# Optimization experiments

Hardware: AMD Instinct MI355X
Metric: run time of the kernel (lower is better)

Reference implementation:

```python
import jax, jax.numpy as jnp
import numpy as np

ROLE_BITS = 20
NHEAD = 16
D_MODEL = 1024
D_KEY = D_MODEL // NHEAD  # 64
D_FIL = 512
DFF = 4096
EPS = 1e-5


def _ln(x, g, b):
    mu = jnp.mean(x, axis=-1, keepdims=True)
    var = jnp.mean(jnp.square(x - mu), axis=-1, keepdims=True)
    return (x - mu) * jax.lax.rsqrt(var + EPS) * g + b


def setup_inputs() -> dict:
    key = jax.random.key(0)
    ks = jax.random.split(key, 10)
    N, BSZ, MEM = 16384, 16, 8
    D_IN = D_FIL + ROLE_BITS  # 532
    values = jax.random.normal(ks[0], (N, D_FIL), jnp.float32)
    role_index = jax.random.randint(ks[1], (N,), 1, 2 ** ROLE_BITS)
    # every (batch, memory_slot) pair occupied -> static shapes (compression is a no-op)
    slot = jax.random.permutation(ks[2], jnp.tile(jnp.arange(BSZ * MEM), N // (BSZ * MEM)))
    batch_index = (slot // MEM).astype(jnp.int32)
    memory_index = (slot % MEM).astype(jnp.int32)
    query_vectors = jax.random.normal(ks[3], (NHEAD, D_KEY), jnp.float32) * (1.0 / np.sqrt(D_KEY))
    s = 0.02
    Wk = jax.random.normal(ks[4], (D_MODEL, D_IN), jnp.float32) * s
    Wv = jax.random.normal(ks[5], (D_MODEL, D_IN), jnp.float32) * s
    Wo = jax.random.normal(ks[6], (D_MODEL, D_MODEL), jnp.float32) * s
    W1 = jax.random.normal(ks[7], (DFF, D_MODEL), jnp.float32) * s
    W2 = jax.random.normal(ks[8], (D_MODEL, DFF), jnp.float32) * s
    return dict(
        values=values, role_index=role_index, batch_index=batch_index,
        memory_index=memory_index, query_vectors=query_vectors,
        Wk=Wk, Wv=Wv, Wo=Wo, bo=jnp.zeros((D_MODEL,), jnp.float32),
        W1=W1, b1=jnp.zeros((DFF,), jnp.float32),
        W2=W2, b2=jnp.zeros((D_MODEL,), jnp.float32),
        g_fil=jnp.ones((D_FIL,), jnp.float32), b_fil=jnp.zeros((D_FIL,), jnp.float32),
        g_mha=jnp.ones((D_IN,), jnp.float32), b_mha=jnp.zeros((D_IN,), jnp.float32),
        g_ff=jnp.ones((D_MODEL,), jnp.float32), b_ff=jnp.zeros((D_MODEL,), jnp.float32),
        g_out=jnp.ones((D_MODEL,), jnp.float32), b_out=jnp.zeros((D_MODEL,), jnp.float32),
        bsz=BSZ, memory_slots=MEM,
    )


def _tree_positional_encodings(role_index):
    # bit-expand role indices: column j is bit j of the role index
    bits = (jnp.bitwise_and(role_index[:, None], 2 ** jnp.arange(ROLE_BITS)) != 0).astype(jnp.float32)
    # locate the highest set bit (torch: flip + argmax)
    mi = jnp.argmax(bits[:, ::-1], axis=1)
    cm = ROLE_BITS - 1 - mi  # index of highest set bit
    bits = bits * (1.0 - jax.nn.one_hot(cm, ROLE_BITS, dtype=bits.dtype))  # zero it out
    branch = jnp.arange(ROLE_BITS)[None, :] < cm[:, None]
    return jnp.where(branch, (bits - 0.5) * 2.0, bits)  # {0,1} -> {-1,1} below MSB


def reference(values, role_index, batch_index, memory_index, query_vectors,
              Wk, Wv, Wo, bo, W1, b1, W2, b2,
              g_fil, b_fil, g_mha, b_mha, g_ff, b_ff, g_out, b_out,
              bsz, memory_slots):
    N = values.shape[0]
    T = bsz * memory_slots  # num_trees (all (batch, slot) pairs occupied)

    tpd = _tree_positional_encodings(role_index)
    x = jnp.concatenate([_ln(values, g_fil, b_fil), tpd], axis=1)  # [N, d_input]
    x = _ln(x, g_mha, b_mha)
    k = (x @ Wk.T).reshape(N, NHEAD, D_KEY)
    v = (x @ Wv.T).reshape(N, NHEAD, D_KEY)
    qkm = jnp.einsum('nhd,hd->nh', k, query_vectors)  # [N, H]

    # combined batch+memory mask: node n attends to flat tree t = b*mem + m
    node_slot = batch_index * memory_slots + memory_index  # [N]
    mask = node_slot[:, None] == jnp.arange(T)[None, :]  # [N, T]
    scores = jnp.where(mask[:, :, None], qkm[:, None, :], -1e9) / np.sqrt(D_KEY)
    attn = jax.nn.softmax(scores, axis=0)  # softmax over nodes, [N, T, H]
    out = jnp.einsum('nhv,nth->thv', v, attn).reshape(T, D_MODEL)

    # post-attention: proj_o + residual with flattened queries, LN, FF, LN
    r1 = (out @ Wo.T + bo) + query_vectors.reshape(-1)
    l1 = _ln(r1, g_ff, b_ff)
    ff = jax.nn.gelu(l1 @ W1.T + b1, approximate=False) @ W2.T + b2
    l2 = _ln(ff + r1, g_out, b_out)

    rectangle_out = l2.reshape(bsz, memory_slots, D_MODEL)
    agent_pad_mask = jnp.zeros((bsz, memory_slots), dtype=bool)
    return rectangle_out, agent_pad_mask
```

## Files before the change

kernel.cpp:

```cpp
#include <hip/hip_runtime.h>
#include <hip/hip_bf16.h>

typedef __hip_bfloat16 bf16;

#define N_NODES 16384
#define D_FIL 512
#define D_IN 532
#define D_MODEL 1024
#define NHEAD 16
#define D_KEY 64
#define DFF 4096
#define NTREE 128
#define MEM_SLOTS 8
#define NODES_PER_TREE 128
#define EPS 1e-5f
#define XSE 544
#define XSU 272
#define CSTR 32
#define BSTR 40

typedef float f32x4 __attribute__((ext_vector_type(4)));
typedef short s16x8 __attribute__((ext_vector_type(8)));

union PackU { uint4 u; s16x8 s; };

__device__ inline float gelu_exact(float x) {
    return 0.5f * x * (1.0f + erff(x * 0.7071067811865476f));
}

__device__ inline void blockReduceSum2_512(float& a, float& b, float* sm) {
    int tid = threadIdx.x;
    int lane = tid & 63, wid = tid >> 6;
#pragma unroll
    for (int off = 32; off > 0; off >>= 1) {
        a += __shfl_down(a, off, 64);
        b += __shfl_down(b, off, 64);
    }
    if (lane == 0) { sm[wid] = a; sm[8 + wid] = b; }
    __syncthreads();
    if (tid == 0) {
        float s0 = 0.f, s1 = 0.f;
#pragma unroll
        for (int i = 0; i < 8; ++i) { s0 += sm[i]; s1 += sm[8 + i]; }
        sm[16] = s0; sm[17] = s1;
    }
    __syncthreads();
    a = sm[16]; b = sm[17];
}

__global__ __launch_bounds__(256) void prep_kernel(
        const float* __restrict__ values, const int* __restrict__ role,
        const int* __restrict__ bidx, const int* __restrict__ midx,
        const float* __restrict__ g_fil, const float* __restrict__ b_fil,
        const float* __restrict__ g_mha, const float* __restrict__ b_mha,
        bf16* __restrict__ xs, int* __restrict__ counts,
        const float* __restrict__ q, const float* __restrict__ Wk,
        unsigned* __restrict__ wqb,
        const float* __restrict__ Wv, float* __restrict__ wvt) {
    int b = blockIdx.x;
    int tid = threadIdx.x;

    if (b < 16) {
        int h = b;
        __shared__ float qs[64];
        if (tid < 64) qs[tid] = q[h * 64 + tid];
        __syncthreads();
        for (int p = tid; p < XSU; p += 256) {
            unsigned out = 0u;
            if (p < 266) {
                float a0 = 0.f, a1 = 0.f;
                int j0 = 2 * p;
#pragma unroll 8
                for (int d = 0; d < 64; ++d) {
                    const float* wr = Wk + (size_t)(h * 64 + d) * D_IN;
                    a0 += qs[d] * wr[j0];
                    a1 += qs[d] * wr[j0 + 1];
                }
                unsigned u0 = (unsigned)__bfloat16_as_ushort(__float2bfloat16(a0));
                unsigned u1 = (unsigned)__bfloat16_as_ushort(__float2bfloat16(a1));
                out = (u1 << 16) | u0;
            }
            wqb[h * XSU + p] = out;
        }
        return;
    }

    if (b < 560) {
        __shared__ float tile[32][33];
        int vb = b - 16;
        int c0 = (vb & 31) * 32, j0 = (vb >> 5) * 32;
        int tx = tid & 31, ty = tid >> 5;
#pragma unroll
        for (int r = 0; r < 4; ++r) {
            int cc = ty + r * 8;
            int j = j0 + tx;
            tile[cc][tx] = (j < D_IN) ? Wv[(size_t)(c0 + cc) * D_IN + j] : 0.f;
        }
        __syncthreads();
#pragma unroll
        for (int r = 0; r < 4; ++r) {
            int j = j0 + ty + r * 8;
            if (j < D_IN) wvt[(size_t)j * D_MODEL + c0 + tx] = tile[tx][ty + r * 8];
        }
        return;
    }

    int wave = tid >> 6;
    int l = tid & 63;
    int n = (b - 560) * 4 + wave;

    const float4* vp = (const float4*)(values + (size_t)n * D_FIL + l * 8);
    float4 v0 = vp[0], v1 = vp[1];

    int row = 0;
    if (l == 0) {
        int slot = bidx[n] * MEM_SLOTS + midx[n];
        int pos = atomicAdd(&counts[slot * CSTR], 1);
        row = slot * NODES_PER_TREE + pos;
    }

    float s = v0.x + v0.y + v0.z + v0.w + v1.x + v1.y + v1.z + v1.w;
    float ss = v0.x * v0.x + v0.y * v0.y + v0.z * v0.z + v0.w * v0.w
             + v1.x * v1.x + v1.y * v1.y + v1.z * v1.z + v1.w * v1.w;
#pragma unroll
    for (int m = 1; m < 64; m <<= 1) {
        s += __shfl_xor(s, m, 64);
        ss += __shfl_xor(ss, m, 64);
    }
    float mu = s * (1.f / D_FIL);
    float var = ss * (1.f / D_FIL) - mu * mu;
    float rs = rsqrtf(var + EPS);

    const float4* gf = (const float4*)(g_fil + l * 8);
    const float4* bf = (const float4*)(b_fil + l * 8);
    float4 gf0 = gf[0], gf1 = gf[1], bf0 = bf[0], bf1 = bf[1];
    float y[8];
    y[0] = (v0.x - mu) * rs * gf0.x + bf0.x;
    y[1] = (v0.y - mu) * rs * gf0.y + bf0.y;
    y[2] = (v0.z - mu) * rs * gf0.z + bf0.z;
    y[3] = (v0.w - mu) * rs * gf0.w + bf0.w;
    y[4] = (v1.x - mu) * rs * gf1.x + bf1.x;
    y[5] = (v1.y - mu) * rs * gf1.y + bf1.y;
    y[6] = (v1.z - mu) * rs * gf1.z + bf1.z;
    y[7] = (v1.w - mu) * rs * gf1.w + bf1.w;

    int r = role[n];
    int cm = 31 - __clz(r);
    float s_t = 2.f * (float)(__popc(r) - 1) - (float)cm;
    float ss_t = (float)cm;

    float s2 = y[0] + y[1] + y[2] + y[3] + y[4] + y[5] + y[6] + y[7];
    float ss2 = y[0] * y[0] + y[1] * y[1] + y[2] * y[2] + y[3] * y[3]
              + y[4] * y[4] + y[5] * y[5] + y[6] * y[6] + y[7] * y[7];
#pragma unroll
    for (int m = 1; m < 64; m <<= 1) {
        s2 += __shfl_xor(s2, m, 64);
        ss2 += __shfl_xor(ss2, m, 64);
    }
    s2 += s_t; ss2 += ss_t;
    float mu2 = s2 * (1.f / D_IN);
    float var2 = ss2 * (1.f / D_IN) - mu2 * mu2;
    float rs2 = rsqrtf(var2 + EPS);

    const float4* gm = (const float4*)(g_mha + l * 8);
    const float4* bm = (const float4*)(b_mha + l * 8);
    float4 gm0 = gm[0], gm1 = gm[1], bm0 = bm[0], bm1 = bm[1];
    float x[8];
    x[0] = (y[0] - mu2) * rs2 * gm0.x + bm0.x;
    x[1] = (y[1] - mu2) * rs2 * gm0.y + bm0.y;
    x[2] = (y[2] - mu2) * rs2 * gm0.z + bm0.z;
    x[3] = (y[3] - mu2) * rs2 * gm0.w + bm0.w;
    x[4] = (y[4] - mu2) * rs2 * gm1.x + bm1.x;
    x[5] = (y[5] - mu2) * rs2 * gm1.y + bm1.y;
    x[6] = (y[6] - mu2) * rs2 * gm1.z + bm1.z;
    x[7] = (y[7] - mu2) * rs2 * gm1.w + bm1.w;

    row = __shfl(row, 0, 64);

    {
        unsigned us[8];
#pragma unroll
        for (int k = 0; k < 8; ++k)
            us[k] = (unsigned)__bfloat16_as_ushort(__float2bfloat16(x[k]));
        uint4 pk = make_uint4((us[1] << 16) | us[0], (us[3] << 16) | us[2],
                              (us[5] << 16) | us[4], (us[7] << 16) | us[6]);
        *(uint4*)((char*)xs + (size_t)row * (XSE * 2) + 16 * l) = pk;
    }

    if (l < 20) {
        int bit = (r >> l) & 1;
        float tpd = (l < cm) ? (bit ? 1.f : -1.f) : 0.f;
        float x2 = (tpd - mu2) * rs2 * g_mha[512 + l] + b_mha[512 + l];
        xs[(size_t)row * XSE + 512 + l] = __float2bfloat16(x2);
    } else if (l < 26) {
        ((unsigned*)xs)[(size_t)row * XSU + 266 + (l - 20)] = 0u;
    }
}

__global__ __launch_bounds__(256) void attn_fused_kernel(const unsigned* __restrict__ xsu,
                                                         const unsigned* __restrict__ wqb,
                                                         const float* __restrict__ wvt,
                                                         float* __restrict__ attn_out) {
    int hg = blockIdx.x, t = blockIdx.y, tid = threadIdx.x;
    __shared__ __align__(16) float a4[NODES_PER_TREE * 4];
    __shared__ __align__(16) char sbuf[8576];
    unsigned* wsh = (unsigned*)sbuf;
    float (*zs)[536] = (float(*)[536])sbuf;

    for (int i = tid; i < 4 * 274; i += 256) {
        int hh = i / 274, p = i - hh * 274;
        wsh[hh * 274 + p] = (p < XSU) ? wqb[(hg * 4 + hh) * XSU + p] : 0u;
    }
    __syncthreads();

    {
        int i = tid >> 2, hh = tid & 3;
        const uint2* xr0 = (const uint2*)(xsu + (size_t)(t * NODES_PER_TREE + i) * XSU);
        const uint2* xr1 = (const uint2*)(xsu + (size_t)(t * NODES_PER_TREE + i + 64) * XSU);
        const uint2* wr  = (const uint2*)(wsh + hh * 274);
        float a0 = 0.f, a1 = 0.f;
#pragma unroll 8
        for (int j = 0; j < 133; ++j) {
            uint2 wu = wr[j];
            uint2 xa = xr0[j];
            uint2 xb = xr1[j];
            float w0 = __uint_as_float(wu.x << 16), w1 = __uint_as_float(wu.x & 0xffff0000u);
            float w2 = __uint_as_float(wu.y << 16), w3 = __uint_as_float(wu.y & 0xffff0000u);
            a0 += __uint_as_float(xa.x << 16) * w0 + __uint_as_float(xa.x & 0xffff0000u) * w1
                + __uint_as_float(xa.y << 16) * w2 + __uint_as_float(xa.y & 0xffff0000u) * w3;
            a1 += __uint_as_float(xb.x << 16) * w0 + __uint_as_float(xb.x & 0xffff0000u) * w1
                + __uint_as_float(xb.y << 16) * w2 + __uint_as_float(xb.y & 0xffff0000u) * w3;
        }
        a4[tid] = a0 * 0.125f;
        a4[tid + 256] = a1 * 0.125f;
    }
    __syncthreads();

    int hh = tid >> 6, lane = tid & 63;
    {
        float s0 = a4[lane * 4 + hh], s1 = a4[(lane + 64) * 4 + hh];
        float m = fmaxf(s0, s1);
#pragma unroll
        for (int off = 32; off > 0; off >>= 1) m = fmaxf(m, __shfl_xor(m, off, 64));
        float e0 = expf(s0 - m), e1 = expf(s1 - m);
        float sum = e0 + e1;
#pragma unroll
        for (int off = 32; off > 0; off >>= 1) sum += __shfl_xor(sum, off, 64);
        float inv = 1.0f / sum;
        a4[lane * 4 + hh] = e0 * inv;
        a4[(lane + 64) * 4 + hh] = e1 * inv;
    }
    __syncthreads();

    {
        bool hasT = tid < 10;
        float az[4][2] = {};
        float at[4][2] = {};
        const unsigned* xt = xsu + (size_t)t * NODES_PER_TREE * XSU;
        for (int i0 = 0; i0 < NODES_PER_TREE; i0 += 8) {
            unsigned u[8], u2[8];
            float4 av[8];
#pragma unroll
            for (int k = 0; k < 8; ++k) u[k] = xt[(size_t)(i0 + k) * XSU + tid];
#pragma unroll
            for (int k = 0; k < 8; ++k) u2[k] = hasT ? xt[(size_t)(i0 + k) * XSU + 256 + tid] : 0u;
#pragma unroll
            for (int k = 0; k < 8; ++k) av[k] = *(const float4*)(a4 + (i0 + k) * 4);
#pragma unroll
            for (int k = 0; k < 8; ++k) {
                float x0 = __uint_as_float(u[k] << 16);
                float x1 = __uint_as_float(u[k] & 0xffff0000u);
                float x2 = __uint_as_float(u2[k] << 16);
                float x3 = __uint_as_float(u2[k] & 0xffff0000u);
                float4 a = av[k];
                az[0][0] += a.x * x0; az[0][1] += a.x * x1;
                az[1][0] += a.y * x0; az[1][1] += a.y * x1;
                az[2][0] += a.z * x0; az[2][1] += a.z * x1;
                az[3][0] += a.w * x0; az[3][1] += a.w * x1;
                at[0][0] += a.x * x2; at[0][1] += a.x * x3;
                at[1][0] += a.y * x2; at[1][1] += a.y * x3;
                at[2][0] += a.z * x2; at[2][1] += a.z * x3;
                at[3][0] += a.w * x2; at[3][1] += a.w * x3;
            }
        }
        __syncthreads();
#pragma unroll
        for (int k = 0; k < 4; ++k) {
            *(float2*)(&zs[k][2 * tid]) = make_float2(az[k][0], az[k][1]);
            if (hasT) *(float2*)(&zs[k][512 + 2 * tid]) = make_float2(at[k][0], at[k][1]);
        }
    }
    __syncthreads();

    int c = hg * 256 + tid;
    const float* wp = wvt + c;
    float acc0 = 0.f, acc1 = 0.f;
    for (int j0 = 0; j0 < 528; j0 += 8) {
        float wv[8];
#pragma unroll
        for (int k = 0; k < 8; ++k) wv[k] = wp[(size_t)(j0 + k) * D_MODEL];
#pragma unroll
        for (int k = 0; k < 8; k += 2) {
            acc0 += zs[hh][j0 + k] * wv[k];
            acc1 += zs[hh][j0 + k + 1] * wv[k + 1];
        }
    }
    {
        float wv[4];
#pragma unroll
        for (int k = 0; k < 4; ++k) wv[k] = wp[(size_t)(528 + k) * D_MODEL];
#pragma unroll
        for (int k = 0; k < 4; k += 2) {
            acc0 += zs[hh][528 + k] * wv[k];
            acc1 += zs[hh][528 + k + 1] * wv[k + 1];
        }
    }
    attn_out[(size_t)t * D_MODEL + c] = acc0 + acc1;
}

__global__ __launch_bounds__(256) void gemm_mfma_sk(const float* __restrict__ A,
                                                    const float* __restrict__ B,
                                                    float* __restrict__ Cpart,
                                                    int N, int K, int nsb) {
    __shared__ __align__(16) unsigned short bhi[32 * BSTR];
    __shared__ __align__(16) unsigned short blo[32 * BSTR];
    int tid = threadIdx.x;
    int col0 = blockIdx.x * 32;
    int k0 = blockIdx.y * nsb * 32;
    float* C = Cpart + (size_t)blockIdx.y * 128 * N;

    int w = tid >> 6, l = tid & 63;
    int l15 = l & 15, l4 = l >> 4;
    int scol = tid >> 3, sk4 = (tid & 7) * 4;

    f32x4 acc[2][2];
#pragma unroll
    for (int rt = 0; rt < 2; ++rt)
#pragma unroll
        for (int ct = 0; ct < 2; ++ct) acc[rt][ct] = (f32x4){0.f, 0.f, 0.f, 0.f};

    for (int s = 0; s < nsb; ++s) {
        int kb = k0 + s * 32;

        const float* bp = B + (size_t)(col0 + scol) * K + kb + sk4;
        float4 fb = *(const float4*)bp;

        float4 fa[2][2];
#pragma unroll
        for (int rt = 0; rt < 2; ++rt) {
            const float* ap = A + (size_t)(32 * w + 16 * rt + l15) * K + kb + l4 * 8;
            fa[rt][0] = *(const float4*)ap;
            fa[rt][1] = *(const float4*)(ap + 4);
        }

        {
            float fe[4] = {fb.x, fb.y, fb.z, fb.w};
            unsigned hu[2], lu[2];
#pragma unroll
            for (int p = 0; p < 2; ++p) {
                unsigned u0 = __float_as_uint(fe[2 * p]);
                unsigned u1 = __float_as_uint(fe[2 * p + 1]);
                unsigned h0 = u0 & 0xffff0000u, h1 = u1 & 0xffff0000u;
                float d0 = fe[2 * p] - __uint_as_float(h0);
                float d1 = fe[2 * p + 1] - __uint_as_float(h1);
                hu[p] = h1 | (u0 >> 16);
                lu[p] = (__float_as_uint(d1) & 0xffff0000u) | (__float_as_uint(d0) >> 16);
            }
            *(uint2*)(&bhi[scol * BSTR + sk4]) = make_uint2(hu[0], hu[1]);
            *(uint2*)(&blo[scol * BSTR + sk4]) = make_uint2(lu[0], lu[1]);
        }
        __syncthreads();

        s16x8 ah[2], al[2];
#pragma unroll
        for (int rt = 0; rt < 2; ++rt) {
            float fe[8] = {fa[rt][0].x, fa[rt][0].y, fa[rt][0].z, fa[rt][0].w,
                           fa[rt][1].x, fa[rt][1].y, fa[rt][1].z, fa[rt][1].w};
            unsigned hu[4], lu[4];
#pragma unroll
            for (int p = 0; p < 4; ++p) {
                unsigned u0 = __float_as_uint(fe[2 * p]);
                unsigned u1 = __float_as_uint(fe[2 * p + 1]);
                unsigned h0 = u0 & 0xffff0000u, h1 = u1 & 0xffff0000u;
                float d0 = fe[2 * p] - __uint_as_float(h0);
                float d1 = fe[2 * p + 1] - __uint_as_float(h1);
                hu[p] = h1 | (u0 >> 16);
                lu[p] = (__float_as_uint(d1) & 0xffff0000u) | (__float_as_uint(d0) >> 16);
            }
            PackU uh, ul;
            uh.u = make_uint4(hu[0], hu[1], hu[2], hu[3]);
            ul.u = make_uint4(lu[0], lu[1], lu[2], lu[3]);
            ah[rt] = uh.s;
            al[rt] = ul.s;
        }

#pragma unroll
        for (int ct = 0; ct < 2; ++ct) {
            PackU rbh, rbl;
            rbh.u = *(const uint4*)(&bhi[(16 * ct + l15) * BSTR + l4 * 8]);
            rbl.u = *(const uint4*)(&blo[(16 * ct + l15) * BSTR + l4 * 8]);
#pragma unroll
            for (int rt = 0; rt < 2; ++rt) {
                acc[rt][ct] = __builtin_amdgcn_mfma_f32_16x16x32_bf16(ah[rt], rbh.s, acc[rt][ct], 0, 0, 0);
                acc[rt][ct] = __builtin_amdgcn_mfma_f32_16x16x32_bf16(al[rt], rbh.s, acc[rt][ct], 0, 0, 0);
                acc[rt][ct] = __builtin_amdgcn_mfma_f32_16x16x32_bf16(ah[rt], rbl.s, acc[rt][ct], 0, 0, 0);
            }
        }
        __syncthreads();
    }

#pragma unroll
    for (int rt = 0; rt < 2; ++rt) {
        int row = 32 * w + 16 * rt + l4 * 4;
#pragma unroll
        for (int ct = 0; ct < 2; ++ct) {
            int col = col0 + 16 * ct + l15;
#pragma unroll
            for (int r = 0; r < 4; ++r)
                C[(size_t)(row + r) * N + col] = acc[rt][ct][r];
        }
    }
}

__global__ __launch_bounds__(512) void ln_r1_kernel(const float* __restrict__ po, const float* __restrict__ bo,
                             const float* __restrict__ qvec, const float* __restrict__ g,
                             const float* __restrict__ b, float* __restrict__ r1,
                             float* __restrict__ l1) {
    int t = blockIdx.x, tid = threadIdx.x;
    __shared__ float sm[18];
    float e[2];
#pragma unroll
    for (int c = 0; c < 2; ++c) {
        int j = c * 512 + tid;
        float v = bo[j] + qvec[j];
#pragma unroll
        for (int s = 0; s < 8; ++s)
            v += po[(size_t)s * NTREE * D_MODEL + (size_t)t * D_MODEL + j];
        e[c] = v;
        r1[(size_t)t * D_MODEL + j] = v;
    }
    float s = e[0] + e[1];
    float ss = e[0] * e[0] + e[1] * e[1];
    blockReduceSum2_512(s, ss, sm);
    float mu = s * (1.f / D_MODEL);
    float var = ss * (1.f / D_MODEL) - mu * mu;
    float rs = rsqrtf(var + EPS);
#pragma unroll
    for (int c = 0; c < 2; ++c) {
        int j = c * 512 + tid;
        l1[(size_t)t * D_MODEL + j] = (e[c] - mu) * rs * g[j] + b[j];
    }
}

__global__ void gelu_reduce_kernel(const float* __restrict__ p1, const float* __restrict__ b1,
                                   float* __restrict__ h1) {
    int idx4 = (blockIdx.x * 256 + threadIdx.x) * 4;
    int col = idx4 & (DFF - 1);
    float4 v = *(const float4*)(b1 + col);
#pragma unroll
    for (int s = 0; s < 4; ++s) {
        float4 p = *(const float4*)(p1 + (size_t)s * NTREE * DFF + idx4);
        v.x += p.x; v.y += p.y; v.z += p.z; v.w += p.w;
    }
    v.x = gelu_exact(v.x); v.y = gelu_exact(v.y);
    v.z = gelu_exact(v.z); v.w = gelu_exact(v.w);
    *(float4*)(h1 + idx4) = v;
}

__global__ __launch_bounds__(512) void ln_out_kernel(const float* __restrict__ p2, const float* __restrict__ b2,
                              const float* __restrict__ r1, const float* __restrict__ g,
                              const float* __restrict__ b, float* __restrict__ out) {
    int t = blockIdx.x, tid = threadIdx.x;
    __shared__ float sm[18];
    float e[2];
#pragma unroll
    for (int c = 0; c < 2; ++c) {
        int j = c * 512 + tid;
        float v = b2[j] + r1[(size_t)t * D_MODEL + j];
#pragma unroll
        for (int s = 0; s < 16; ++s)
            v += p2[(size_t)s * NTREE * D_MODEL + (size_t)t * D_MODEL + j];
        e[c] = v;
    }
    float s = e[0] + e[1];
    float ss = e[0] * e[0] + e[1] * e[1];
    blockReduceSum2_512(s, ss, sm);
    float mu = s * (1.f / D_MODEL);
    float var = ss * (1.f / D_MODEL) - mu * mu;
    float rs = rsqrtf(var + EPS);
#pragma unroll
    for (int c = 0; c < 2; ++c) {
        int j = c * 512 + tid;
        out[(size_t)t * D_MODEL + j] = (e[c] - mu) * rs * g[j] + b[j];
    }
    if (t == 0 && tid < 128) out[(size_t)NTREE * D_MODEL + tid] = 0.f;
}

extern "C" void kernel_launch(void* const* d_in, const int* in_sizes, int n_in,
                              void* d_out, int out_size, void* d_ws, size_t ws_size,
                              hipStream_t stream) {
    const float* values = (const float*)d_in[0];
    const int* role     = (const int*)d_in[1];
    const int* bidx     = (const int*)d_in[2];
    const int* midx     = (const int*)d_in[3];
    const float* qvec   = (const float*)d_in[4];
    const float* Wk     = (const float*)d_in[5];
    const float* Wv     = (const float*)d_in[6];
    const float* Wo     = (const float*)d_in[7];
    const float* bo     = (const float*)d_in[8];
    const float* W1     = (const float*)d_in[9];
    const float* b1     = (const float*)d_in[10];
    const float* W2     = (const float*)d_in[11];
    const float* b2     = (const float*)d_in[12];
    const float* g_fil  = (const float*)d_in[13];
    const float* b_fil  = (const float*)d_in[14];
    const float* g_mha  = (const float*)d_in[15];
    const float* b_mha  = (const float*)d_in[16];
    const float* g_ff   = (const float*)d_in[17];
    const float* b_ff   = (const float*)d_in[18];
    const float* g_out  = (const float*)d_in[19];
    const float* b_out  = (const float*)d_in[20];

    char* w = (char*)d_ws;
    int*   counts   = (int*)(w + 0);
    unsigned* wqb   = (unsigned*)(w + 16384);
    float* attn_out = (float*)(w + 34816);
    float* r1       = (float*)(w + 559104);
    float* l1       = (float*)(w + 1083392);
    float* h1       = (float*)(w + 1607680);
    float* wvt      = (float*)(w + 3704832);
    char*  big      = w + 5883904;
    bf16*  xs = (bf16*)big;
    float* po = (float*)big;
    float* p1 = (float*)(big + 4194304);
    float* p2 = (float*)big;

    float* out = (float*)d_out;

    hipMemsetAsync(counts, 0, 16384, stream);

    prep_kernel<<<4656, 256, 0, stream>>>(values, role, bidx, midx,
                                          g_fil, b_fil, g_mha, b_mha,
                                          xs, counts,
                                          qvec, Wk, wqb, Wv, wvt);

    attn_fused_kernel<<<dim3(4, NTREE), 256, 0, stream>>>((const unsigned*)xs, wqb, wvt, attn_out);

    gemm_mfma_sk<<<dim3(32, 8), 256, 0, stream>>>(attn_out, Wo, po, D_MODEL, D_MODEL, 4);

    ln_r1_kernel<<<NTREE, 512, 0, stream>>>(po, bo, qvec, g_ff, b_ff, r1, l1);

    gemm_mfma_sk<<<dim3(128, 4), 256, 0, stream>>>(l1, W1, p1, DFF, D_MODEL, 8);

    gelu_reduce_kernel<<<512, 256, 0, stream>>>(p1, b1, h1);

    gemm_mfma_sk<<<dim3(32, 16), 256, 0, stream>>>(h1, W2, p2, D_MODEL, DFF, 8);

    ln_out_kernel<<<NTREE, 512, 0, stream>>>(p2, b2, r1, g_out, b_out, out);
}
```

Before: 236.6 us.

## Double attention kernel block size and remap blocks so trees share an XCD

The fused attention kernel now runs 512 threads per block. Each thread computes one score, the weighted value sum is split across two node halves and reduced in shared memory, and the Wv projection is split across two K halves. The 1D grid is remapped so the four head-groups of a tree land on the same XCD, which should improve L2 reuse of that tree's activations. The cost is more shared memory, extra barriers and reduction passes, and idle threads during the softmax.

```diff
diff --git a/kernel.cpp b/kernel.cpp
--- a/kernel.cpp
+++ b/kernel.cpp
@@ -197,17 +197,21 @@
     }
 }
 
-__global__ __launch_bounds__(256) void attn_fused_kernel(const unsigned* __restrict__ xsu,
+__global__ __launch_bounds__(512) void attn_fused_kernel(const unsigned* __restrict__ xsu,
                                                          const unsigned* __restrict__ wqb,
                                                          const float* __restrict__ wvt,
                                                          float* __restrict__ attn_out) {
-    int hg = blockIdx.x, t = blockIdx.y, tid = threadIdx.x;
+    int f = blockIdx.x;
+    int xcd = f & 7, slot = f >> 3;
+    int hg = slot & 3;
+    int t = (slot >> 2) * 8 + xcd;
+    int tid = threadIdx.x;
+
     __shared__ __align__(16) float a4[NODES_PER_TREE * 4];
-    __shared__ __align__(16) char sbuf[8576];
-    unsigned* wsh = (unsigned*)sbuf;
-    float (*zs)[536] = (float(*)[536])sbuf;
-
-    for (int i = tid; i < 4 * 274; i += 256) {
+    __shared__ __align__(16) unsigned wsh[4 * 274];
+    __shared__ __align__(16) float zsb[2][4][536];
+
+    for (int i = tid; i < 4 * 274; i += 512) {
         int hh = i / 274, p = i - hh * 274;
         wsh[hh * 274 + p] = (p < XSU) ? wqb[(hg * 4 + hh) * XSU + p] : 0u;
     }
@@ -215,29 +219,24 @@
 
     {
         int i = tid >> 2, hh = tid & 3;
-        const uint2* xr0 = (const uint2*)(xsu + (size_t)(t * NODES_PER_TREE + i) * XSU);
-        const uint2* xr1 = (const uint2*)(xsu + (size_t)(t * NODES_PER_TREE + i + 64) * XSU);
-        const uint2* wr  = (const uint2*)(wsh + hh * 274);
-        float a0 = 0.f, a1 = 0.f;
+        const uint2* xr = (const uint2*)(xsu + (size_t)(t * NODES_PER_TREE + i) * XSU);
+        const uint2* wr = (const uint2*)(wsh + hh * 274);
+        float a0 = 0.f;
 #pragma unroll 8
         for (int j = 0; j < 133; ++j) {
             uint2 wu = wr[j];
-            uint2 xa = xr0[j];
-            uint2 xb = xr1[j];
+            uint2 xa = xr[j];
             float w0 = __uint_as_float(wu.x << 16), w1 = __uint_as_float(wu.x & 0xffff0000u);
             float w2 = __uint_as_float(wu.y << 16), w3 = __uint_as_float(wu.y & 0xffff0000u);
             a0 += __uint_as_float(xa.x << 16) * w0 + __uint_as_float(xa.x & 0xffff0000u) * w1
                 + __uint_as_float(xa.y << 16) * w2 + __uint_as_float(xa.y & 0xffff0000u) * w3;
-            a1 += __uint_as_float(xb.x << 16) * w0 + __uint_as_float(xb.x & 0xffff0000u) * w1
-                + __uint_as_float(xb.y << 16) * w2 + __uint_as_float(xb.y & 0xffff0000u) * w3;
         }
         a4[tid] = a0 * 0.125f;
-        a4[tid + 256] = a1 * 0.125f;
-    }
-    __syncthreads();
-
-    int hh = tid >> 6, lane = tid & 63;
-    {
+    }
+    __syncthreads();
+
+    if (tid < 256) {
+        int hh = tid >> 6, lane = tid & 63;
         float s0 = a4[lane * 4 + hh], s1 = a4[(lane + 64) * 4 + hh];
         float m = fmaxf(s0, s1);
 #pragma unroll
@@ -253,19 +252,21 @@
     __syncthreads();
 
     {
-        bool hasT = tid < 10;
+        int half = tid >> 8;
+        int colu = tid & 255;
+        bool hasT = colu < 10;
         float az[4][2] = {};
         float at[4][2] = {};
-        const unsigned* xt = xsu + (size_t)t * NODES_PER_TREE * XSU;
-        for (int i0 = 0; i0 < NODES_PER_TREE; i0 += 8) {
+        const unsigned* xt = xsu + (size_t)(t * NODES_PER_TREE + half * 64) * XSU;
+        for (int i0 = 0; i0 < 64; i0 += 8) {
             unsigned u[8], u2[8];
             float4 av[8];
 #pragma unroll
-            for (int k = 0; k < 8; ++k) u[k] = xt[(size_t)(i0 + k) * XSU + tid];
-#pragma unroll
-            for (int k = 0; k < 8; ++k) u2[k] = hasT ? xt[(size_t)(i0 + k) * XSU + 256 + tid] : 0u;
-#pragma unroll
-            for (int k = 0; k < 8; ++k) av[k] = *(const float4*)(a4 + (i0 + k) * 4);
+            for (int k = 0; k < 8; ++k) u[k] = xt[(size_t)(i0 + k) * XSU + colu];
+#pragma unroll
+            for (int k = 0; k < 8; ++k) u2[k] = hasT ? xt[(size_t)(i0 + k) * XSU + 256 + colu] : 0u;
+#pragma unroll
+            for (int k = 0; k < 8; ++k) av[k] = *(const float4*)(a4 + (half * 64 + i0 + k) * 4);
 #pragma unroll
             for (int k = 0; k < 8; ++k) {
                 float x0 = __uint_as_float(u[k] << 16);
@@ -283,39 +284,46 @@
                 at[3][0] += a.w * x2; at[3][1] += a.w * x3;
             }
         }
-        __syncthreads();
 #pragma unroll
         for (int k = 0; k < 4; ++k) {
-            *(float2*)(&zs[k][2 * tid]) = make_float2(az[k][0], az[k][1]);
-            if (hasT) *(float2*)(&zs[k][512 + 2 * tid]) = make_float2(at[k][0], at[k][1]);
-        }
-    }
-    __syncthreads();
-
-    int c = hg * 256 + tid;
-    const float* wp = wvt + c;
-    float acc0 = 0.f, acc1 = 0.f;
-    for (int j0 = 0; j0 < 528; j0 += 8) {
-        float wv[8];
-#pragma unroll
-        for (int k = 0; k < 8; ++k) wv[k] = wp[(size_t)(j0 + k) * D_MODEL];
-#pragma unroll
-        for (int k = 0; k < 8; k += 2) {
-            acc0 += zs[hh][j0 + k] * wv[k];
-            acc1 += zs[hh][j0 + k + 1] * wv[k + 1];
-        }
-    }
+            *(float2*)(&zsb[half][k][2 * colu]) = make_float2(az[k][0], az[k][1]);
+            if (hasT) *(float2*)(&zsb[half][k][512 + 2 * colu]) = make_float2(at[k][0], at[k][1]);
+        }
+    }
+    __syncthreads();
+
     {
-        float wv[4];
-#pragma unroll
-        for (int k = 0; k < 4; ++k) wv[k] = wp[(size_t)(528 + k) * D_MODEL];
-#pragma unroll
-        for (int k = 0; k < 4; k += 2) {
-            acc0 += zs[hh][528 + k] * wv[k];
-            acc1 += zs[hh][528 + k + 1] * wv[k + 1];
-        }
-    }
-    attn_out[(size_t)t * D_MODEL + c] = acc0 + acc1;
+        float* z0 = &zsb[0][0][0];
+        const float* z1 = &zsb[1][0][0];
+        for (int idx = tid; idx < 4 * 536; idx += 512) z0[idx] += z1[idx];
+    }
+    __syncthreads();
+
+    {
+        int cc = tid & 255, jh = tid >> 8;
+        int hh = cc >> 6;
+        const float* wp = wvt + hg * 256 + cc;
+        const float* zp = &zsb[0][hh][0];
+        int jbeg = jh ? 264 : 0;
+        int jend = jh ? 532 : 264;
+        float acc0 = 0.f, acc1 = 0.f;
+        int j0 = jbeg;
+        for (; j0 + 8 <= jend; j0 += 8) {
+            float wv[8];
+#pragma unroll
+            for (int k = 0; k < 8; ++k) wv[k] = wp[(size_t)(j0 + k) * D_MODEL];
+#pragma unroll
+            for (int k = 0; k < 8; k += 2) {
+                acc0 += zp[j0 + k] * wv[k];
+                acc1 += zp[j0 + k + 1] * wv[k + 1];
+            }
+        }
+        for (; j0 < jend; ++j0) acc0 += zp[j0] * wp[(size_t)j0 * D_MODEL];
+        a4[tid] = acc0 + acc1;
+    }
+    __syncthreads();
+    if (tid < 256)
+        attn_out[(size_t)t * D_MODEL + hg * 256 + tid] = a4[tid] + a4[tid + 256];
 }
 
 __global__ __launch_bounds__(256) void gemm_mfma_sk(const float* __restrict__ A,
@@ -544,7 +552,7 @@
                                           xs, counts,
                                           qvec, Wk, wqb, Wv, wvt);
 
-    attn_fused_kernel<<<dim3(4, NTREE), 256, 0, stream>>>((const unsigned*)xs, wqb, wvt, attn_out);
+    attn_fused_kernel<<<512, 512, 0, stream>>>((const unsigned*)xs, wqb, wvt, attn_out);
 
     gemm_mfma_sk<<<dim3(32, 8), 256, 0, stream>>>(attn_out, Wo, po, D_MODEL, D_MODEL, 4);
 
```

Result: slower. 343.0 us (+45.0%).
